# Kernel tuning notes

Hardware: AMD Instinct MI355X
Metric: run time of the kernel (lower is better)

## Reference

```python
import jax, jax.numpy as jnp
import numpy as np

EPS = 1e-7
MAX_NORM = 1.0 - 1e-3  # projection radius of the unit Poincare ball (c=1)
ALPHA = 0.2            # LeakyReLU negative slope
NEG_INF = -9e15


def _proj(x, max_norm=MAX_NORM):
    # Project points back inside the Poincare ball along the last dim.
    norm = jnp.clip(jnp.linalg.norm(x, axis=-1, keepdims=True), EPS)
    return jnp.where(norm > max_norm, x / norm * max_norm, x)


def _logmap0(x):
    # Log map at the origin of the Poincare ball, c = 1.
    norm = jnp.clip(jnp.linalg.norm(x, axis=-1, keepdims=True), EPS, 1.0 - EPS)
    return jnp.arctanh(norm) * x / norm


def _expmap0(v):
    # Exp map at the origin of the Poincare ball, c = 1.
    norm = jnp.clip(jnp.linalg.norm(v, axis=-1, keepdims=True), EPS)
    return jnp.tanh(norm) * v / norm


def setup_inputs() -> dict:
    key = jax.random.key(0)
    k1, k2, k3 = jax.random.split(key, 3)
    N, D = 12288, 128
    # points strictly inside the ball: ||x|| ~ 0.01*sqrt(128) ~ 0.11 < 1
    x = jax.random.normal(k1, (N, D), dtype=jnp.float32) * 0.01
    adj = jax.random.randint(k2, (N, N), 0, 2, dtype=jnp.int32)
    # attention vector a, as in init: N(0, 0.2) then proj(a, 0.9) row-wise
    a = jax.random.normal(k3, (2 * D, 1), dtype=jnp.float32) * 0.2
    a = _proj(a, 0.9)
    return {"x": x, "adj": adj, "a": a}


def reference(x, adj, a):
    D = a.shape[0] // 2
    x_tan = _logmap0(x)                       # [N, D]
    wh1 = x_tan @ a[:D]                       # [N, 1]
    wh2 = x_tan @ a[D:]                       # [N, 1]
    e = jax.nn.leaky_relu(wh1 + wh2.T, ALPHA)  # [N, N] additive scores
    scores = jnp.where(adj > 0, e, NEG_INF)
    attention = jax.nn.softmax(scores, axis=1)  # dropout omitted (eval mode)
    x_tan_prime = attention @ x_tan            # [N, D]
    return _proj(_expmap0(x_tan_prime))
```

## Files before the change

kernel.cpp:

```cpp
#include <hip/hip_runtime.h>
#include <math.h>

#define NN 12288
#define DD 128
#define EPSF 1e-7f
#define MAXNORM (1.0f - 1e-3f)
#define CSPLIT 4
#define CCOLS (NN / CSPLIT)
#define CSTEPS (CCOLS / 128)
#define SLABS (CSTEPS / 4)

typedef __attribute__((ext_vector_type(8))) short short8_t;
typedef __attribute__((ext_vector_type(4))) float float4_t;
typedef unsigned short ushort_t;

__device__ __forceinline__ unsigned short f2bf(float f) {
    unsigned int u = __builtin_bit_cast(unsigned int, f);
    unsigned int r = u + 0x7FFFu + ((u >> 16) & 1u);
    return (unsigned short)(r >> 16);
}

__global__ __launch_bounds__(128) void prep_kernel(
    const float* __restrict__ x, const float* __restrict__ a,
    ushort_t* __restrict__ xtb,
    float* __restrict__ wh1, float* __restrict__ wh2)
{
    const int r = blockIdx.x;
    const int t = threadIdx.x;
    const float xv = x[r * DD + t];
    const float a1 = a[t];
    const float a2 = a[DD + t];
    float s0 = xv * xv, s1 = xv * a1, s2 = xv * a2;
    #pragma unroll
    for (int o = 32; o > 0; o >>= 1) {
        s0 += __shfl_xor(s0, o);
        s1 += __shfl_xor(s1, o);
        s2 += __shfl_xor(s2, o);
    }
    __shared__ float red[6];
    const int w = t >> 6;
    if ((t & 63) == 0) { red[w * 3 + 0] = s0; red[w * 3 + 1] = s1; red[w * 3 + 2] = s2; }
    __syncthreads();
    const float sumsq = red[0] + red[3];
    const float d1    = red[1] + red[4];
    const float d2    = red[2] + red[5];
    const float nraw  = sqrtf(sumsq);
    const float nrm   = fminf(fmaxf(nraw, EPSF), 1.0f - EPSF);
    const float scale = atanhf(nrm) / nrm;
    xtb[(size_t)r * DD + t] = f2bf(xv * scale);
    if (t == 0) {
        wh1[r] = scale * d1;
        wh2[r] = scale * d2;
    }
}

__global__ __launch_bounds__(256) void swizzle_kernel(
    const ushort_t* __restrict__ xtb, ushort_t* __restrict__ xtB)
{
    __shared__ ushort_t raw[32 * 136];
    const int C = blockIdx.x;
    const int t = threadIdx.x;
    #pragma unroll
    for (int p = 0; p < 2; ++p) {
        const int idx = p * 256 + t;
        const int j = idx >> 4, cell = idx & 15;
        const uint4 v = *(const uint4*)(xtb + (size_t)(C * 32 + j) * DD + cell * 8);
        *(uint4*)&raw[j * 136 + cell * 8] = v;
    }
    __syncthreads();
    #pragma unroll
    for (int p = 0; p < 2; ++p) {
        const int oc = p * 256 + t;
        const int dt = oc >> 6;
        const int l6 = oc & 63;
        const int l15 = l6 & 15, q = l6 >> 4;
        short8_t v;
        #pragma unroll
        for (int e = 0; e < 8; ++e)
            v[e] = (short)raw[(q * 8 + e) * 136 + dt * 16 + l15];
        *(short8_t*)(xtB + (size_t)C * 4096 + oc * 8) = v;
    }
}

__global__ __launch_bounds__(256, 1) void attn_kernel(
    const int* __restrict__ adj,
    const ushort_t* __restrict__ xtB,
    const float* __restrict__ wh1, const float* __restrict__ wh2,
    float* __restrict__ pout, float* __restrict__ plsum)
{
    __shared__ __align__(16) ushort_t B_lds[512 * DD];
    __shared__ __align__(16) float wh2_lds[CCOLS];

    const int t = threadIdx.x;
    const int w = t >> 6, lane = t & 63;
    const int l15 = lane & 15, quad = lane >> 4;
    const int cy = blockIdx.y;
    const int jcol0 = cy * CCOLS;
    const int rowbase = blockIdx.x * 64 + w * 16;

    #pragma unroll
    for (int m = 0; m < CCOLS / 256; ++m)
        wh2_lds[m * 256 + t] = wh2[jcol0 + m * 256 + t];
    const float wh1i = wh1[rowbase + l15];

    const int* adj_lane = adj + (size_t)(rowbase + l15) * NN + jcol0 + quad * 8;
    const uint4* Bsrc = (const uint4*)(xtB + (size_t)(jcol0 >> 5) * 4096);

    float4_t acc[8];
    #pragma unroll
    for (int dt = 0; dt < 8; ++dt) acc[dt] = (float4_t)0.0f;
    float lsum = 0.0f;

    int4 Ra[8], Rb[8];

    auto adj_load = [&](int st, int4 (&A)[8]) {
        const int* bp = adj_lane + st * 128;
        #pragma unroll
        for (int kc = 0; kc < 4; ++kc) {
            A[kc * 2 + 0] = *(const int4*)(bp + kc * 32);
            A[kc * 2 + 1] = *(const int4*)(bp + kc * 32 + 4);
        }
    };

    auto stage = [&](int sl) {
        const uint4* gp = Bsrc + (size_t)sl * 8192 + (size_t)w * 64 + lane;
        char* lb = (char*)B_lds + (size_t)w * 64 * 16;
        #pragma unroll
        for (int m = 0; m < 32; ++m) {
            __builtin_amdgcn_global_load_lds(
                (const __attribute__((address_space(1))) unsigned int*)(gp + m * 256),
                (__attribute__((address_space(3))) unsigned int*)(lb + (size_t)m * 256 * 16),
                16, 0, 0);
        }
    };

    auto compute = [&](int st, int q, const int4 (&A)[8]) {
        #pragma unroll
        for (int kc = 0; kc < 4; ++kc) {
            const int4 Av = A[kc * 2 + 0], Ac = A[kc * 2 + 1];
            const int wbase = st * 128 + kc * 32 + quad * 8;
            const float4 Wa = *(const float4*)&wh2_lds[wbase];
            const float4 Wb = *(const float4*)&wh2_lds[wbase + 4];
            const float u0 = wh1i + Wa.x, u1 = wh1i + Wa.y;
            const float u2 = wh1i + Wa.z, u3 = wh1i + Wa.w;
            const float u4 = wh1i + Wb.x, u5 = wh1i + Wb.y;
            const float u6 = wh1i + Wb.z, u7 = wh1i + Wb.w;
            const float p0 = (Av.x > 0) ? __expf(fmaxf(u0, 0.2f * u0)) : 0.0f;
            const float p1 = (Av.y > 0) ? __expf(fmaxf(u1, 0.2f * u1)) : 0.0f;
            const float p2 = (Av.z > 0) ? __expf(fmaxf(u2, 0.2f * u2)) : 0.0f;
            const float p3 = (Av.w > 0) ? __expf(fmaxf(u3, 0.2f * u3)) : 0.0f;
            const float p4 = (Ac.x > 0) ? __expf(fmaxf(u4, 0.2f * u4)) : 0.0f;
            const float p5 = (Ac.y > 0) ? __expf(fmaxf(u5, 0.2f * u5)) : 0.0f;
            const float p6 = (Ac.z > 0) ? __expf(fmaxf(u6, 0.2f * u6)) : 0.0f;
            const float p7 = (Ac.w > 0) ? __expf(fmaxf(u7, 0.2f * u7)) : 0.0f;
            lsum += ((p0 + p1) + (p2 + p3)) + ((p4 + p5) + (p6 + p7));
            short8_t af;
            af[0] = (short)f2bf(p0); af[1] = (short)f2bf(p1);
            af[2] = (short)f2bf(p2); af[3] = (short)f2bf(p3);
            af[4] = (short)f2bf(p4); af[5] = (short)f2bf(p5);
            af[6] = (short)f2bf(p6); af[7] = (short)f2bf(p7);
            const ushort_t* Bp = B_lds + (q * 4 + kc) * 4096 + lane * 8;
            #pragma unroll
            for (int dt = 0; dt < 8; ++dt) {
                const short8_t Bf = *(const short8_t*)(Bp + dt * 512);
                acc[dt] = __builtin_amdgcn_mfma_f32_16x16x32_bf16(af, Bf, acc[dt], 0, 0, 0);
            }
        }
    };

    adj_load(0, Ra);
    adj_load(1, Rb);

    #pragma unroll 1
    for (int sl = 0; sl < SLABS; ++sl) {
        const int st0 = sl * 4;
        __syncthreads();
        stage(sl);
        __syncthreads();
        compute(st0 + 0, 0, Ra);
        if (st0 + 2 < CSTEPS) adj_load(st0 + 2, Ra);
        compute(st0 + 1, 1, Rb);
        if (st0 + 3 < CSTEPS) adj_load(st0 + 3, Rb);
        compute(st0 + 2, 2, Ra);
        if (st0 + 4 < CSTEPS) adj_load(st0 + 4, Ra);
        compute(st0 + 3, 3, Rb);
        if (st0 + 5 < CSTEPS) adj_load(st0 + 5, Rb);
    }

    float v = lsum;
    v += __shfl_xor(v, 16);
    v += __shfl_xor(v, 32);
    if (quad == 0) plsum[(size_t)cy * NN + rowbase + l15] = v;
    #pragma unroll
    for (int dt = 0; dt < 8; ++dt)
        #pragma unroll
        for (int reg = 0; reg < 4; ++reg)
            pout[((size_t)cy * NN + rowbase + quad * 4 + reg) * DD + dt * 16 + l15]
                = acc[dt][reg];
}

__global__ __launch_bounds__(128) void reduce_kernel(
    const float* __restrict__ pout, const float* __restrict__ plsum,
    float* __restrict__ out)
{
    const int i = blockIdx.x;
    const int t = threadIdx.x;
    float v = 0.0f;
    #pragma unroll
    for (int s = 0; s < CSPLIT; ++s) v += pout[((size_t)s * NN + i) * DD + t];
    float ls = 0.0f;
    #pragma unroll
    for (int s = 0; s < CSPLIT; ++s) ls += plsum[(size_t)s * NN + i];
    v /= ls;
    float ss = v * v;
    #pragma unroll
    for (int o = 1; o < 64; o <<= 1) ss += __shfl_xor(ss, o);
    __shared__ float r2[2];
    if ((t & 63) == 0) r2[t >> 6] = ss;
    __syncthreads();
    const float total = r2[0] + r2[1];
    const float nraw = sqrtf(total);
    const float nv   = fmaxf(nraw, EPSF);
    const float th   = tanhf(nv);
    const float ysc  = th / nv;
    const float nyr  = ysc * nraw;
    const float ny   = fmaxf(nyr, EPSF);
    const float psc  = (ny > MAXNORM) ? (MAXNORM / ny) : 1.0f;
    const float os   = ysc * psc;
    out[(size_t)i * DD + t] = v * os;
}

extern "C" void kernel_launch(void* const* d_in, const int* in_sizes, int n_in,
                              void* d_out, int out_size, void* d_ws, size_t ws_size,
                              hipStream_t stream) {
    const float* x   = (const float*)d_in[0];
    const int*   adj = (const int*)d_in[1];
    const float* a   = (const float*)d_in[2];
    float* out = (float*)d_out;

    char* ws = (char*)d_ws;
    ushort_t* xtb = (ushort_t*)ws;  ws += (size_t)NN * DD * sizeof(ushort_t);
    ushort_t* xtB = (ushort_t*)ws;  ws += (size_t)NN * DD * sizeof(ushort_t);
    float* wh1 = (float*)ws;        ws += NN * sizeof(float);
    float* wh2 = (float*)ws;        ws += NN * sizeof(float);
    float* plsum = (float*)ws;      ws += (size_t)CSPLIT * NN * sizeof(float);
    float* pout  = (float*)ws;

    prep_kernel<<<NN, 128, 0, stream>>>(x, a, xtb, wh1, wh2);
    swizzle_kernel<<<NN / 32, 256, 0, stream>>>(xtb, xtB);
    attn_kernel<<<dim3(NN / 64, CSPLIT), 256, 0, stream>>>(
        adj, xtB, wh1, wh2, pout, plsum);
    reduce_kernel<<<NN, 128, 0, stream>>>(pout, plsum, out);
}
```

Baseline: 857.2 us.

## Halve LDS slab and compress adjacency to bitmasks for two blocks per CU

Doubles the column split so each block handles half as many columns, halves the LDS B-slab to 256 rows, and raises the launch bound to two blocks per CU. The double-buffered int4 adjacency registers are replaced by one register set plus a 32-bit bitmask per step, which frees VGPRs so occupancy can increase and better hide adj load latency. The cost is twice as many partial output rows for the reduce kernel to read and sum, more frequent barriers per column, and less distance between prefetch and use.

Result: faster. 830.6 us (-3.1%).

```diff
diff --git a/kernel.cpp b/kernel.cpp
--- a/kernel.cpp
+++ b/kernel.cpp
@@ -5,10 +5,10 @@
 #define DD 128
 #define EPSF 1e-7f
 #define MAXNORM (1.0f - 1e-3f)
-#define CSPLIT 4
+#define CSPLIT 8
 #define CCOLS (NN / CSPLIT)
 #define CSTEPS (CCOLS / 128)
-#define SLABS (CSTEPS / 4)
+#define SLABS (CSTEPS / 2)
 
 typedef __attribute__((ext_vector_type(8))) short short8_t;
 typedef __attribute__((ext_vector_type(4))) float float4_t;
@@ -82,13 +82,13 @@
     }
 }
 
-__global__ __launch_bounds__(256, 1) void attn_kernel(
+__global__ __launch_bounds__(256, 2) void attn_kernel(
     const int* __restrict__ adj,
     const ushort_t* __restrict__ xtB,
     const float* __restrict__ wh1, const float* __restrict__ wh2,
     float* __restrict__ pout, float* __restrict__ plsum)
 {
-    __shared__ __align__(16) ushort_t B_lds[512 * DD];
+    __shared__ __align__(16) ushort_t B_lds[256 * DD];
     __shared__ __align__(16) float wh2_lds[CCOLS];
 
     const int t = threadIdx.x;
@@ -111,22 +111,40 @@
     for (int dt = 0; dt < 8; ++dt) acc[dt] = (float4_t)0.0f;
     float lsum = 0.0f;
 
-    int4 Ra[8], Rb[8];
-
-    auto adj_load = [&](int st, int4 (&A)[8]) {
+    int4 R[8];
+    unsigned mCur;
+
+    auto adj_load = [&](int st) {
         const int* bp = adj_lane + st * 128;
         #pragma unroll
         for (int kc = 0; kc < 4; ++kc) {
-            A[kc * 2 + 0] = *(const int4*)(bp + kc * 32);
-            A[kc * 2 + 1] = *(const int4*)(bp + kc * 32 + 4);
-        }
+            R[kc * 2 + 0] = *(const int4*)(bp + kc * 32);
+            R[kc * 2 + 1] = *(const int4*)(bp + kc * 32 + 4);
+        }
+    };
+
+    auto compress = [&]() -> unsigned {
+        unsigned m = 0;
+        #pragma unroll
+        for (int kc = 0; kc < 4; ++kc) {
+            const int4 a0 = R[kc * 2 + 0], a1 = R[kc * 2 + 1];
+            m |= (a0.x > 0 ? 1u : 0u) << (kc * 8 + 0);
+            m |= (a0.y > 0 ? 1u : 0u) << (kc * 8 + 1);
+            m |= (a0.z > 0 ? 1u : 0u) << (kc * 8 + 2);
+            m |= (a0.w > 0 ? 1u : 0u) << (kc * 8 + 3);
+            m |= (a1.x > 0 ? 1u : 0u) << (kc * 8 + 4);
+            m |= (a1.y > 0 ? 1u : 0u) << (kc * 8 + 5);
+            m |= (a1.z > 0 ? 1u : 0u) << (kc * 8 + 6);
+            m |= (a1.w > 0 ? 1u : 0u) << (kc * 8 + 7);
+        }
+        return m;
     };
 
     auto stage = [&](int sl) {
-        const uint4* gp = Bsrc + (size_t)sl * 8192 + (size_t)w * 64 + lane;
+        const uint4* gp = Bsrc + (size_t)sl * 4096 + (size_t)w * 64 + lane;
         char* lb = (char*)B_lds + (size_t)w * 64 * 16;
         #pragma unroll
-        for (int m = 0; m < 32; ++m) {
+        for (int m = 0; m < 16; ++m) {
             __builtin_amdgcn_global_load_lds(
                 (const __attribute__((address_space(1))) unsigned int*)(gp + m * 256),
                 (__attribute__((address_space(3))) unsigned int*)(lb + (size_t)m * 256 * 16),
@@ -134,10 +152,10 @@
         }
     };
 
-    auto compute = [&](int st, int q, const int4 (&A)[8]) {
+    auto compute = [&](int st, int par, unsigned mask) {
         #pragma unroll
         for (int kc = 0; kc < 4; ++kc) {
-            const int4 Av = A[kc * 2 + 0], Ac = A[kc * 2 + 1];
+            const unsigned wq = (mask >> (kc * 8)) & 0xFFu;
             const int wbase = st * 128 + kc * 32 + quad * 8;
             const float4 Wa = *(const float4*)&wh2_lds[wbase];
             const float4 Wb = *(const float4*)&wh2_lds[wbase + 4];
@@ -145,21 +163,21 @@
             const float u2 = wh1i + Wa.z, u3 = wh1i + Wa.w;
             const float u4 = wh1i + Wb.x, u5 = wh1i + Wb.y;
             const float u6 = wh1i + Wb.z, u7 = wh1i + Wb.w;
-            const float p0 = (Av.x > 0) ? __expf(fmaxf(u0, 0.2f * u0)) : 0.0f;
-            const float p1 = (Av.y > 0) ? __expf(fmaxf(u1, 0.2f * u1)) : 0.0f;
-            const float p2 = (Av.z > 0) ? __expf(fmaxf(u2, 0.2f * u2)) : 0.0f;
-            const float p3 = (Av.w > 0) ? __expf(fmaxf(u3, 0.2f * u3)) : 0.0f;
-            const float p4 = (Ac.x > 0) ? __expf(fmaxf(u4, 0.2f * u4)) : 0.0f;
-            const float p5 = (Ac.y > 0) ? __expf(fmaxf(u5, 0.2f * u5)) : 0.0f;
-            const float p6 = (Ac.z > 0) ? __expf(fmaxf(u6, 0.2f * u6)) : 0.0f;
-            const float p7 = (Ac.w > 0) ? __expf(fmaxf(u7, 0.2f * u7)) : 0.0f;
+            const float p0 = (wq & 1u)   ? __expf(fmaxf(u0, 0.2f * u0)) : 0.0f;
+            const float p1 = (wq & 2u)   ? __expf(fmaxf(u1, 0.2f * u1)) : 0.0f;
+            const float p2 = (wq & 4u)   ? __expf(fmaxf(u2, 0.2f * u2)) : 0.0f;
+            const float p3 = (wq & 8u)   ? __expf(fmaxf(u3, 0.2f * u3)) : 0.0f;
+            const float p4 = (wq & 16u)  ? __expf(fmaxf(u4, 0.2f * u4)) : 0.0f;
+            const float p5 = (wq & 32u)  ? __expf(fmaxf(u5, 0.2f * u5)) : 0.0f;
+            const float p6 = (wq & 64u)  ? __expf(fmaxf(u6, 0.2f * u6)) : 0.0f;
+            const float p7 = (wq & 128u) ? __expf(fmaxf(u7, 0.2f * u7)) : 0.0f;
             lsum += ((p0 + p1) + (p2 + p3)) + ((p4 + p5) + (p6 + p7));
             short8_t af;
             af[0] = (short)f2bf(p0); af[1] = (short)f2bf(p1);
             af[2] = (short)f2bf(p2); af[3] = (short)f2bf(p3);
             af[4] = (short)f2bf(p4); af[5] = (short)f2bf(p5);
             af[6] = (short)f2bf(p6); af[7] = (short)f2bf(p7);
-            const ushort_t* Bp = B_lds + (q * 4 + kc) * 4096 + lane * 8;
+            const ushort_t* Bp = B_lds + (par * 4 + kc) * 4096 + lane * 8;
             #pragma unroll
             for (int dt = 0; dt < 8; ++dt) {
                 const short8_t Bf = *(const short8_t*)(Bp + dt * 512);
@@ -168,23 +186,24 @@
         }
     };
 
-    adj_load(0, Ra);
-    adj_load(1, Rb);
+    adj_load(0);
+    mCur = compress();
+    adj_load(1);
 
     #pragma unroll 1
     for (int sl = 0; sl < SLABS; ++sl) {
-        const int st0 = sl * 4;
+        const int st0 = sl * 2;
         __syncthreads();
         stage(sl);
         __syncthreads();
-        compute(st0 + 0, 0, Ra);
-        if (st0 + 2 < CSTEPS) adj_load(st0 + 2, Ra);
-        compute(st0 + 1, 1, Rb);
-        if (st0 + 3 < CSTEPS) adj_load(st0 + 3, Rb);
-        compute(st0 + 2, 2, Ra);
-        if (st0 + 4 < CSTEPS) adj_load(st0 + 4, Ra);
-        compute(st0 + 3, 3, Rb);
-        if (st0 + 5 < CSTEPS) adj_load(st0 + 5, Rb);
+        compute(st0 + 0, 0, mCur);
+        mCur = compress();
+        if (st0 + 2 < CSTEPS) adj_load(st0 + 2);
+        compute(st0 + 1, 1, mCur);
+        if (st0 + 2 < CSTEPS) {
+            mCur = compress();
+            if (st0 + 3 < CSTEPS) adj_load(st0 + 3);
+        }
     }
 
     float v = lsum;
```
